# Kernel optimization log

Hardware: AMD Instinct MI355X
Metric: run time of the kernel (lower is better)

## Reference

```python
import jax, jax.numpy as jnp
import numpy as np

B, C, H, W = 16, 256, 96, 96
CQ = C // 8      # 32, query/key channels in CrossAttention
CM = C // 2      # 128, inter_planes


def conv1x1(x, w, b=None):
    # x: [B,Cin,H,W], w: [Cout,Cin]
    y = jnp.einsum('bchw,oc->bohw', x, w)
    if b is not None:
        y = y + b[None, :, None, None]
    return y


def cross_attention(x, wq, bq, wk, bk, wv, bv, gamma):
    # criss-cross (axial H and W) attention with -inf diagonal on the H branch
    b_, c_, h_, w_ = x.shape
    q = conv1x1(x, wq, bq)  # [B,CQ,H,W]
    k = conv1x1(x, wk, bk)
    v = conv1x1(x, wv, bv)  # [B,C,H,W]
    # energy over column (H axis): [B,H,W,H], masked diag h==h'
    e_h = jnp.einsum('bchw,bckw->bhwk', q, k)
    diag = jnp.eye(h_, dtype=bool)[None, :, None, :]  # [1,H,1,H]
    e_h = jnp.where(diag, -jnp.inf, e_h)
    # energy over row (W axis): [B,H,W,W]
    e_w = jnp.einsum('bchw,bchv->bhwv', q, k)
    att = jax.nn.softmax(jnp.concatenate([e_h, e_w], axis=3), axis=3)
    a_h, a_w = att[..., :h_], att[..., h_:]
    out_h = jnp.einsum('bckw,bhwk->bchw', v, a_h)
    out_w = jnp.einsum('bchv,bhwv->bchw', v, a_w)
    return gamma * (out_h + out_w) + x


def spatial_weighted(x, w_q_right, w_v_right, w_up, b_up):
    b_, _, h_, w_ = x.shape
    inp = conv1x1(x, w_v_right).reshape(b_, CM, h_ * w_)        # [B,CM,HW]
    mask = conv1x1(x, w_q_right).reshape(b_, 1, h_ * w_)        # [B,1,HW]
    mask = jax.nn.softmax(mask, axis=2)
    ctx = jnp.einsum('bcn,bon->bco', inp, mask)                 # [B,CM,1]
    ctx = jnp.einsum('bci,oc->boi', ctx, w_up) + b_up[None, :, None]  # [B,C,1]
    mask_ch = jax.nn.sigmoid(ctx)[..., None]                    # [B,C,1,1]
    return x * mask_ch


def channel_weighted(x, w_q_left, w_v_left):
    b_, _, h_, w_ = x.shape
    g = conv1x1(x, w_q_left)                                    # [B,CM,H,W]
    avg = jnp.mean(g, axis=(2, 3))                              # [B,CM]
    theta = conv1x1(x, w_v_left).reshape(b_, CM, h_ * w_)       # [B,CM,HW]
    ctx = jnp.einsum('bc,bcn->bn', avg, theta)                  # [B,HW]
    ctx = jax.nn.softmax(ctx, axis=1).reshape(b_, 1, h_, w_)
    return x * jax.nn.sigmoid(ctx)


def setup_inputs() -> dict:
    key = jax.random.key(0)
    ks = jax.random.split(key, 16)
    s = lambda fan_in: (2.0 / fan_in) ** 0.5
    inp = {
        'x': jax.random.normal(ks[0], (B, C, H, W), jnp.float32),
        'w_q_right': jax.random.normal(ks[1], (1, C), jnp.float32) * s(C),
        'w_v_right': jax.random.normal(ks[2], (CM, C), jnp.float32) * s(C),
        'w_up': jax.random.normal(ks[3], (C, CM), jnp.float32) * s(CM),
        'b_up': jnp.zeros((C,), jnp.float32),
        'w_q_left': jax.random.normal(ks[4], (CM, C), jnp.float32) * s(C),
        'w_v_left': jax.random.normal(ks[5], (CM, C), jnp.float32) * s(C),
        'cr_wq': jax.random.normal(ks[6], (CQ, C), jnp.float32) * s(C),
        'cr_bq': jnp.zeros((CQ,), jnp.float32),
        'cr_wk': jax.random.normal(ks[7], (CQ, C), jnp.float32) * s(C),
        'cr_bk': jnp.zeros((CQ,), jnp.float32),
        'cr_wv': jax.random.normal(ks[8], (C, C), jnp.float32) * s(C),
        'cr_bv': jnp.zeros((C,), jnp.float32),
        'gamma': jax.random.normal(ks[9], (1,), jnp.float32) * 0.1,
    }
    return inp


def reference(x, w_q_right, w_v_right, w_up, b_up, w_q_left, w_v_left,
              cr_wq, cr_bq, cr_wk, cr_bk, cr_wv, cr_bv, gamma):
    cross = lambda t: cross_attention(t, cr_wq, cr_bq, cr_wk, cr_bk, cr_wv, cr_bv, gamma)
    ctx_channel = cross(spatial_weighted(x, w_q_right, w_v_right, w_up, b_up))
    ctx_spatial = cross(channel_weighted(x, w_q_left, w_v_left))
    return cross(ctx_spatial + ctx_channel)
```

## Files before the change

kernel.cpp:

```cpp
#include <hip/hip_runtime.h>
#include <math.h>

#define Bn 16
#define Cn 256
#define CQn 32
#define CMn 128
#define Hn 96
#define Wn 96
#define Nn 9216
#define PIXn 147456

typedef short bf8 __attribute__((ext_vector_type(8)));
typedef float f32x4 __attribute__((ext_vector_type(4)));
#define MFMA(a,b,c) __builtin_amdgcn_mfma_f32_16x16x32_bf16(a,b,c,0,0,0)

typedef unsigned short ushort_t;
typedef _Float16 h16;

__device__ inline ushort_t f2bf(float f){
  union{float f; unsigned int u;} v; v.f=f;
  unsigned int r = v.u + 0x7fffu + ((v.u>>16)&1u);
  return (ushort_t)(r>>16);
}
__device__ inline float bf2f(ushort_t s){
  union{unsigned int u; float f;} v; v.u = ((unsigned int)s)<<16;
  return v.f;
}
__device__ inline ushort_t f2h(float f){
  union{h16 h; ushort_t u;} v; v.h=(h16)f; return v.u;
}
__device__ inline float h2f(ushort_t u){
  union{ushort_t u; h16 h;} v; v.u=u; return (float)v.h;
}

__device__ inline float waveSum(float v){
#pragma unroll
  for(int o=32;o;o>>=1) v += __shfl_down(v,o,64);
  return v;
}
__device__ inline float waveMax(float v){
#pragma unroll
  for(int o=32;o;o>>=1) v = fmaxf(v,__shfl_down(v,o,64));
  return v;
}


__global__ __launch_bounds__(1024) void k_pass1(const float* __restrict__ x,
    const float* __restrict__ wqr, float* __restrict__ xmean,
    float* __restrict__ partp){
  int cg = blockIdx.x, b = blockIdx.y, tid = threadIdx.x;
  __shared__ float r16[16];
  float mp[9];
#pragma unroll
  for(int k=0;k<9;k++) mp[k]=0.f;
  for(int cc=0;cc<16;cc++){
    int c = cg*16+cc;
    const float* row = x + ((size_t)b*Cn + c)*Nn;
    float w = wqr[c];
    float s = 0.f;
#pragma unroll
    for(int k=0;k<9;k++){
      float v = row[k*1024+tid];
      s += v;
      mp[k] += w*v;
    }
    s = waveSum(s);
    if((tid&63)==0) r16[tid>>6]=s;
    __syncthreads();
    if(tid==0){
      float t=0.f;
      for(int i=0;i<16;i++) t+=r16[i];
      xmean[(size_t)b*Cn + c] = t*(1.f/Nn);
    }
    __syncthreads();
  }
  float* dst = partp + ((size_t)cg*Bn + b)*Nn;
#pragma unroll
  for(int k=0;k<9;k++) dst[k*1024+tid]=mp[k];
}

__global__ __launch_bounds__(1024) void k_pass2(const float* __restrict__ x,
    const float* __restrict__ wvec, const float* __restrict__ maskb,
    float* __restrict__ xw, float* __restrict__ partp){
  int cg = blockIdx.x, b = blockIdx.y, tid = threadIdx.x;
  __shared__ float r16[16];
  float cp[9], mk[9];
#pragma unroll
  for(int k=0;k<9;k++){
    cp[k]=0.f;
    mk[k]=maskb[(size_t)b*Nn + k*1024+tid];
  }
  for(int cc=0;cc<16;cc++){
    int c = cg*16+cc;
    const float* row = x + ((size_t)b*Cn + c)*Nn;
    float w = wvec[(size_t)b*Cn + c];
    float s = 0.f;
#pragma unroll
    for(int k=0;k<9;k++){
      float v = row[k*1024+tid];
      s += mk[k]*v;
      cp[k] += w*v;
    }
    s = waveSum(s);
    if((tid&63)==0) r16[tid>>6]=s;
    __syncthreads();
    if(tid==0){
      float t=0.f;
      for(int i=0;i<16;i++) t+=r16[i];
      xw[(size_t)b*Cn + c] = t;
    }
    __syncthreads();
  }
  float* dst = partp + ((size_t)cg*Bn + b)*Nn;
#pragma unroll
  for(int k=0;k<9;k++) dst[k*1024+tid]=cp[k];
}

__global__ void k_red16(const float* __restrict__ part, float* __restrict__ out){
  size_t p = (size_t)blockIdx.x*256 + threadIdx.x;
  float s=0.f;
#pragma unroll
  for(int cg=0;cg<16;cg++) s += part[(size_t)cg*Bn*Nn + p];
  out[p]=s;
}

__global__ void k_small1(const float* __restrict__ xmean, const float* __restrict__ wql,
                         const float* __restrict__ wvl, float* __restrict__ wvec){
  int b=blockIdx.x, t=threadIdx.x;
  __shared__ float xm[Cn];
  __shared__ float av[CMn];
  xm[t] = xmean[b*Cn+t];
  __syncthreads();
  if(t<CMn){
    float s=0.f;
    for(int c=0;c<Cn;c++) s += wql[t*Cn+c]*xm[c];
    av[t]=s;
  }
  __syncthreads();
  float s=0.f;
  for(int m=0;m<CMn;m++) s += av[m]*wvl[m*Cn+t];
  wvec[b*Cn+t]=s;
}

__global__ void k_softmax_n(const float* __restrict__ in, float* __restrict__ out, int mode){
  int b=blockIdx.x, tid=threadIdx.x, lane=tid&63, wid=tid>>6;
  const float* p = in + (size_t)b*Nn;
  __shared__ float red[16];
  __shared__ float bc2[2];
  float mx=-3e38f;
  for(int i=tid;i<Nn;i+=1024) mx=fmaxf(mx,p[i]);
  mx = waveMax(mx);
  if(lane==0) red[wid]=mx;
  __syncthreads();
  if(tid==0){ float m=red[0]; for(int i=1;i<16;i++) m=fmaxf(m,red[i]); bc2[0]=m; }
  __syncthreads();
  mx=bc2[0];
  float s=0.f;
  for(int i=tid;i<Nn;i+=1024) s+=expf(p[i]-mx);
  s = waveSum(s);
  __syncthreads();
  if(lane==0) red[wid]=s;
  __syncthreads();
  if(tid==0){ float t=0.f; for(int i=0;i<16;i++) t+=red[i]; bc2[1]=t; }
  __syncthreads();
  float inv=1.f/bc2[1];
  for(int i=tid;i<Nn;i+=1024){
    float e=expf(p[i]-mx)*inv;
    out[(size_t)b*Nn+i] = mode ? 1.f/(1.f+expf(-e)) : e;
  }
}

__global__ void k_small2(const float* __restrict__ xw, const float* __restrict__ wvr,
                         const float* __restrict__ wup, const float* __restrict__ bup,
                         float* __restrict__ g1){
  int b=blockIdx.x, t=threadIdx.x;
  __shared__ float xs[Cn];
  __shared__ float cx[CMn];
  xs[t]=xw[b*Cn+t];
  __syncthreads();
  if(t<CMn){
    float s=0.f;
    for(int c=0;c<Cn;c++) s += wvr[t*Cn+c]*xs[c];
    cx[t]=s;
  }
  __syncthreads();
  float s=bup[t];
  for(int m=0;m<CMn;m++) s += wup[t*CMn+m]*cx[m];
  g1[b*Cn+t]=1.f/(1.f+expf(-s));
}

__global__ void k_gates(const float* __restrict__ x, const float* __restrict__ g1,
                        const float* __restrict__ m2, ushort_t* __restrict__ t1,
                        ushort_t* __restrict__ t2){
  size_t i4 = ((size_t)blockIdx.x*256 + threadIdx.x)*4;
  int n  = (int)(i4 % Nn);
  int bc = (int)(i4 / Nn);
  int b  = bc / Cn;
  float4 xv = *(const float4*)&x[i4];
  float g = g1[bc];
  float4 mv = *(const float4*)&m2[(size_t)b*Nn + n];
  uint2 a, c;
  a.x = (unsigned)f2bf(xv.x*g) | ((unsigned)f2bf(xv.y*g)<<16);
  a.y = (unsigned)f2bf(xv.z*g) | ((unsigned)f2bf(xv.w*g)<<16);
  c.x = (unsigned)f2bf(xv.x*mv.x) | ((unsigned)f2bf(xv.y*mv.y)<<16);
  c.y = (unsigned)f2bf(xv.z*mv.z) | ((unsigned)f2bf(xv.w*mv.w)<<16);
  *(uint2*)&t1[i4] = a;
  *(uint2*)&t2[i4] = c;
}


__global__ void k_packb(const float* __restrict__ wq, const float* __restrict__ bq,
                        const float* __restrict__ wk, const float* __restrict__ bk,
                        const float* __restrict__ wv, const float* __restrict__ bv,
                        ushort_t* __restrict__ Wp, float* __restrict__ bp){
  int o = blockIdx.x, t = threadIdx.x;
  const float* src; float bs;
  if(o<32){ src = wq + o*Cn; bs = bq[o]; }
  else if(o<64){ src = wk + (o-32)*Cn; bs = bk[o-32]; }
  else { src = wv + (o-64)*Cn; bs = bv[o-64]; }
  Wp[o*Cn+t] = f2bf(src[t]);
  if(t==0) bp[o] = bs;
}

#define AP 40
#define BP 264
#define GP 68

__global__ __launch_bounds__(256) void k_gemm_qkv(const ushort_t* __restrict__ x,
    const ushort_t* __restrict__ Wp, const float* __restrict__ bp,
    ushort_t* __restrict__ Yqk, ushort_t* __restrict__ Vb){
  __shared__ ushort_t SM[320*AP + 64*BP];
  ushort_t* Ws = SM;
  ushort_t* Bt = SM + 320*AP;
  int b  = blockIdx.y;
  int n0 = blockIdx.x*64;
  int tid = threadIdx.x, lane = tid&63, wid = tid>>6;

  {
    const ushort_t* xb = x + (size_t)b*Cn*Nn + n0 + (tid&63);
    int cg = (tid>>6)*8;
#pragma unroll
    for(int p=0;p<8;p++){
      int c8 = p*32 + cg;
      unsigned e0=xb[(size_t)(c8+0)*Nn], e1=xb[(size_t)(c8+1)*Nn];
      unsigned e2=xb[(size_t)(c8+2)*Nn], e3=xb[(size_t)(c8+3)*Nn];
      unsigned e4=xb[(size_t)(c8+4)*Nn], e5=xb[(size_t)(c8+5)*Nn];
      unsigned e6=xb[(size_t)(c8+6)*Nn], e7=xb[(size_t)(c8+7)*Nn];
      uint4 pk;
      pk.x = e0 | (e1<<16); pk.y = e2 | (e3<<16);
      pk.z = e4 | (e5<<16); pk.w = e6 | (e7<<16);
      *(uint4*)&Bt[(tid&63)*BP + c8] = pk;
    }
  }

  f32x4 acc[5][4];
#pragma unroll
  for(int f=0;f<5;f++)
#pragma unroll
    for(int g=0;g<4;g++) acc[f][g] = (f32x4){0.f,0.f,0.f,0.f};

  for(int ki=0;ki<8;ki++){
    __syncthreads();
#pragma unroll
    for(int q=0;q<5;q++){
      int fidx = q*256 + tid;
      int o = fidx>>2, kk = (fidx&3)*8;
      uint4 wv = *(const uint4*)&Wp[o*Cn + ki*32 + kk];
      *(uint4*)&Ws[o*AP + kk] = wv;
    }
    __syncthreads();
    bf8 bfr[4];
#pragma unroll
    for(int g=0;g<4;g++)
      bfr[g] = *(const bf8*)&Bt[(g*16 + (lane&15))*BP + ki*32 + (lane>>4)*8];
#pragma unroll
    for(int f=0;f<5;f++){
      bf8 a = *(const bf8*)&Ws[(wid*80 + f*16 + (lane&15))*AP + (lane>>4)*8];
#pragma unroll
      for(int g=0;g<4;g++) acc[f][g] = MFMA(a, bfr[g], acc[f][g]);
    }
  }

  __syncthreads();
#pragma unroll
  for(int f=0;f<5;f++){
    int o = wid*80 + f*16 + (lane>>4)*4;
#pragma unroll
    for(int i=0;i<4;i++){
      float bias = bp[o+i];
#pragma unroll
      for(int g=0;g<4;g++)
        SM[(o+i)*GP + g*16 + (lane&15)] = f2bf(acc[f][g][i] + bias);
    }
  }
  __syncthreads();
  for(int u=tid; u<320*8; u+=256){
    int lo_ = u>>3, c8 = (u&7)*8;
    ushort_t* dst = (lo_<64) ? (Yqk + ((size_t)b*64 + lo_)*Nn)
                             : (Vb + ((size_t)b*Cn + (lo_-64))*Nn);
    *(uint4*)&dst[n0 + c8] = *(uint4*)&SM[lo_*GP + c8];
  }
}

__global__ __launch_bounds__(256) void k_transpose_b(const ushort_t* __restrict__ src,
                                                     ushort_t* __restrict__ dst){
  __shared__ ushort_t Ls[96*98];
  size_t base = (size_t)blockIdx.x * Nn;
  int tid = threadIdx.x;
  for(int e=tid*2; e<Nn; e+=512){
    unsigned int u = *(const unsigned int*)&src[base+e];
    int r=e/96, c=e%96;
    *(unsigned int*)&Ls[r*98+c] = u;
  }
  __syncthreads();
  for(int e=tid*2; e<Nn; e+=512){
    int r=e/96, c=e%96;
    unsigned int u = (unsigned int)Ls[c*98+r] | (((unsigned int)Ls[(c+1)*98+r])<<16);
    *(unsigned int*)&dst[base+e] = u;
  }
}

__global__ __launch_bounds__(256) void k_e2(const ushort_t* __restrict__ Yqk,
    const ushort_t* __restrict__ Yqkt, ushort_t* __restrict__ attl,
    ushort_t* __restrict__ attr){
  __shared__ ushort_t Qt[96*AP];
  __shared__ ushort_t Kt[96*AP];
  int r = blockIdx.x, mode = blockIdx.y, b = blockIdx.z;
  const ushort_t* Y = mode ? Yqk : Yqkt;
  int pm   = mode ? 1  : 96;
  int pr   = mode ? 96 : 1;
  ushort_t* attx = mode ? attr : attl;
  int tid = threadIdx.x, lane = tid&63, wid = tid>>6;
  {
    int half = tid>>7;
    int cg   = (tid>>5)&3;
    int l32  = tid&31;
    ushort_t* T = half ? Kt : Qt;
    const ushort_t* S = Y + ((size_t)b*64 + half*32 + cg*8)*Nn + (size_t)r*96;
#pragma unroll
    for(int p=0;p<3;p++){
      int sp = p*32 + l32;
      unsigned e0=S[(size_t)0*Nn+sp], e1=S[(size_t)1*Nn+sp];
      unsigned e2=S[(size_t)2*Nn+sp], e3=S[(size_t)3*Nn+sp];
      unsigned e4=S[(size_t)4*Nn+sp], e5=S[(size_t)5*Nn+sp];
      unsigned e6=S[(size_t)6*Nn+sp], e7=S[(size_t)7*Nn+sp];
      uint4 pk;
      pk.x = e0 | (e1<<16); pk.y = e2 | (e3<<16);
      pk.z = e4 | (e5<<16); pk.w = e6 | (e7<<16);
      *(uint4*)&T[sp*AP + cg*8] = pk;
    }
  }
  __syncthreads();
  int mb = (wid>>1)*48, nb = (wid&1)*48;
  const f32x4 z4 = {0.f,0.f,0.f,0.f};
  f32x4 acc[3][3];
  bf8 a[3], bb[3];
#pragma unroll
  for(int f=0;f<3;f++) a[f] = *(const bf8*)&Qt[(mb+f*16+(lane&15))*AP + (lane>>4)*8];
#pragma unroll
  for(int g=0;g<3;g++) bb[g] = *(const bf8*)&Kt[(nb+g*16+(lane&15))*AP + (lane>>4)*8];
#pragma unroll
  for(int f=0;f<3;f++)
#pragma unroll
    for(int g=0;g<3;g++) acc[f][g] = MFMA(a[f], bb[g], z4);
#pragma unroll
  for(int f=0;f<3;f++)
#pragma unroll
    for(int i=0;i<4;i++){
      int m = mb + f*16 + (lane>>4)*4 + i;
      ushort_t* arow = attx + ((size_t)b*Nn + (size_t)m*pm + (size_t)r*pr)*96;
#pragma unroll
      for(int g=0;g<3;g++){
        int n = nb + g*16 + (lane&15);
        arow[n] = f2h(acc[f][g][i]);
      }
    }
}

__global__ void k_softmax_att(const ushort_t* __restrict__ attl,
    const ushort_t* __restrict__ attr,
    ushort_t* __restrict__ attw, ushort_t* __restrict__ atth){
  int wave = threadIdx.x>>6, lane = threadIdx.x&63;
  int p = blockIdx.x*4 + wave;
  const ushort_t* al = attl + (size_t)p*96;
  const ushort_t* ar = attr + (size_t)p*96;
  int b = p/Nn, rem = p%Nn, h = rem/96, w = rem%96;
  float v0 = h2f(al[lane]);
  if(lane==h) v0 = -1e30f;
  float v1;
  if(lane<32){
    v1 = h2f(al[64+lane]);
    if(64+lane==h) v1 = -1e30f;
  } else {
    v1 = h2f(ar[lane-32]);
  }
  float v2 = h2f(ar[lane+32]);
  float mx = fmaxf(v0, fmaxf(v1,v2));
#pragma unroll
  for(int o=32;o;o>>=1) mx = fmaxf(mx, __shfl_xor(mx,o,64));
  float e0=expf(v0-mx), e1=expf(v1-mx), e2=expf(v2-mx);
  float s=e0+e1+e2;
#pragma unroll
  for(int o=32;o;o>>=1) s += __shfl_xor(s,o,64);
  float inv=1.f/s;
  ushort_t* ph = atth + ((size_t)b*Nn + (size_t)w*96 + h)*96;
  ushort_t* pw = attw + (size_t)p*96;
  ph[lane] = f2bf(e0*inv);
  if(lane<32) ph[64+lane] = f2bf(e1*inv);
  else        pw[lane-32] = f2bf(e1*inv);
  pw[lane+32] = f2bf(e2*inv);
}

#define SP 120
#define RP 100

template<int OUTF>
__global__ __launch_bounds__(256) void k_pv2(const ushort_t* __restrict__ Vb,
    const ushort_t* __restrict__ VT, const ushort_t* __restrict__ attw,
    const ushort_t* __restrict__ atth, const ushort_t* resid,
    float* __restrict__ Of, ushort_t* OwB, ushort_t* OT,
    const float* __restrict__ gp){
  __shared__ ushort_t SMEM[128*RP];
  int r = blockIdx.x, mode = blockIdx.y>>1, half = blockIdx.y&1, b = blockIdx.z;
  float gm = gp[0];
  int tid = threadIdx.x, lane = tid&63, wid = tid>>6;
  const ushort_t* V = mode ? VT : Vb;
  size_t vbase = (size_t)b*Cn*Nn + (size_t)r*96;
  bf8 vf[6];
#pragma unroll
  for(int f=0;f<2;f++)
#pragma unroll
    for(int j=0;j<3;j++)
      vf[f*3+j] = *(const bf8*)&V[vbase
        + (size_t)(half*128 + wid*32 + f*16 + (lane&15))*Nn + j*32 + (lane>>4)*8];
  const ushort_t* ab = (mode ? atth : attw) + ((size_t)b*Nn + (size_t)r*96)*96;
  for(int u=tid; u<96*12; u+=256){
    int n=u/12, j8=(u%12)*8;
    uint4 q = *(const uint4*)&ab[n*96 + j8];
    *(uint4*)&SMEM[n*SP + j8] = q;
  }
  __syncthreads();
  f32x4 acc[2][6];
#pragma unroll
  for(int f=0;f<2;f++)
#pragma unroll
    for(int g=0;g<6;g++) acc[f][g] = (f32x4){0.f,0.f,0.f,0.f};
#pragma unroll
  for(int j0=0;j0<3;j0++){
    bf8 bfr[6];
#pragma unroll
    for(int g=0;g<6;g++)
      bfr[g] = *(const bf8*)&SMEM[(g*16+(lane&15))*SP + j0*32 + (lane>>4)*8];
#pragma unroll
    for(int f=0;f<2;f++)
#pragma unroll
      for(int g=0;g<6;g++) acc[f][g] = MFMA(vf[f*3+j0], bfr[g], acc[f][g]);
  }
  __syncthreads();
#pragma unroll
  for(int f=0;f<2;f++){
    int lr = wid*32 + f*16 + (lane>>4)*4;
#pragma unroll
    for(int i=0;i<4;i++)
#pragma unroll
      for(int g=0;g<6;g++)
        SMEM[(lr+i)*RP + g*16 + (lane&15)] = f2bf(gm*acc[f][g][i]);
  }
  __syncthreads();
  for(int u=tid; u<128*12; u+=256){
    int lc = u/12, q8 = (u%12)*8;
    size_t row = vbase + (size_t)(half*128 + lc)*Nn;
    uint4 v = *(uint4*)&SMEM[lc*RP + q8];
    if(mode){
      *(uint4*)&OT[row + q8] = v;
    } else {
      uint4 rv = *(const uint4*)&resid[row + q8];
      unsigned* vp=(unsigned*)&v; unsigned* rp=(unsigned*)&rv;
      if(OUTF){
        float4 o1, o2;
        o1.x = bf2f((ushort_t)(vp[0]&0xffff)) + bf2f((ushort_t)(rp[0]&0xffff));
        o1.y = bf2f((ushort_t)(vp[0]>>16))    + bf2f((ushort_t)(rp[0]>>16));
        o1.z = bf2f((ushort_t)(vp[1]&0xffff)) + bf2f((ushort_t)(rp[1]&0xffff));
        o1.w = bf2f((ushort_t)(vp[1]>>16))    + bf2f((ushort_t)(rp[1]>>16));
        o2.x = bf2f((ushort_t)(vp[2]&0xffff)) + bf2f((ushort_t)(rp[2]&0xffff));
        o2.y = bf2f((ushort_t)(vp[2]>>16))    + bf2f((ushort_t)(rp[2]>>16));
        o2.z = bf2f((ushort_t)(vp[3]&0xffff)) + bf2f((ushort_t)(rp[3]&0xffff));
        o2.w = bf2f((ushort_t)(vp[3]>>16))    + bf2f((ushort_t)(rp[3]>>16));
        *(float4*)&Of[row + q8]     = o1;
        *(float4*)&Of[row + q8 + 4] = o2;
      } else {
        uint4 o;
        unsigned* op=(unsigned*)&o;
#pragma unroll
        for(int k=0;k<4;k++){
          float lo = bf2f((ushort_t)(vp[k]&0xffff)) + bf2f((ushort_t)(rp[k]&0xffff));
          float hi = bf2f((ushort_t)(vp[k]>>16))    + bf2f((ushort_t)(rp[k]>>16));
          op[k] = (unsigned)f2bf(lo) | ((unsigned)f2bf(hi)<<16);
        }
        *(uint4*)&OwB[row + q8] = o;
      }
    }
  }
}

template<int VAR>
__global__ __launch_bounds__(256) void k_merge(float* __restrict__ outf,
    ushort_t* __restrict__ outb, const ushort_t* __restrict__ add,
    const ushort_t* __restrict__ OT){
  __shared__ ushort_t Ls[96*98];
  size_t base = (size_t)blockIdx.x * Nn;
  int tid = threadIdx.x;
  for(int e=tid*2; e<Nn; e+=512){
    unsigned int u = *(const unsigned int*)&OT[base+e];
    int r=e/96, c=e%96;
    *(unsigned int*)&Ls[r*98+c] = u;
  }
  __syncthreads();
  for(int e=tid*4; e<Nn; e+=1024){
    int r=e/96, c=e%96;
    float t0 = bf2f(Ls[(c+0)*98+r]), t1 = bf2f(Ls[(c+1)*98+r]);
    float t2 = bf2f(Ls[(c+2)*98+r]), t3 = bf2f(Ls[(c+3)*98+r]);
    if(VAR==1){
      float4 o = *(float4*)&outf[base+e];
      o.x += t0; o.y += t1; o.z += t2; o.w += t3;
      *(float4*)&outf[base+e] = o;
    } else {
      uint2 u = *(uint2*)&outb[base+e];
      float a0 = bf2f((ushort_t)(u.x&0xffff)) + t0;
      float a1 = bf2f((ushort_t)(u.x>>16))    + t1;
      float a2 = bf2f((ushort_t)(u.y&0xffff)) + t2;
      float a3 = bf2f((ushort_t)(u.y>>16))    + t3;
      if(VAR==2){
        uint2 v = *(const uint2*)&add[base+e];
        a0 += bf2f((ushort_t)(v.x&0xffff));
        a1 += bf2f((ushort_t)(v.x>>16));
        a2 += bf2f((ushort_t)(v.y&0xffff));
        a3 += bf2f((ushort_t)(v.y>>16));
      }
      u.x = (unsigned)f2bf(a0) | ((unsigned)f2bf(a1)<<16);
      u.y = (unsigned)f2bf(a2) | ((unsigned)f2bf(a3)<<16);
      *(uint2*)&outb[base+e] = u;
    }
  }
}

extern "C" void kernel_launch(void* const* d_in, const int* in_sizes, int n_in,
                              void* d_out, int out_size, void* d_ws, size_t ws_size,
                              hipStream_t stream){
  const float* x    = (const float*)d_in[0];
  const float* wqr  = (const float*)d_in[1];
  const float* wvr  = (const float*)d_in[2];
  const float* wup  = (const float*)d_in[3];
  const float* bup  = (const float*)d_in[4];
  const float* wql  = (const float*)d_in[5];
  const float* wvl  = (const float*)d_in[6];
  const float* crwq = (const float*)d_in[7];
  const float* crbq = (const float*)d_in[8];
  const float* crwk = (const float*)d_in[9];
  const float* crbk = (const float*)d_in[10];
  const float* crwv = (const float*)d_in[11];
  const float* crbv = (const float*)d_in[12];
  const float* gma  = (const float*)d_in[13];
  float* out = (float*)d_out;

  const size_t XSZ = (size_t)Bn*Cn*Nn;
  const size_t YSZ = (size_t)Bn*64*Nn;
  char* wsb = (char*)d_ws;
  ushort_t* T1   = (ushort_t*)wsb; wsb += XSZ*2;
  ushort_t* T2   = (ushort_t*)wsb; wsb += XSZ*2;
  ushort_t* Vb   = (ushort_t*)wsb; wsb += XSZ*2;
  ushort_t* VT   = (ushort_t*)wsb; wsb += XSZ*2;
  ushort_t* Yqk  = (ushort_t*)wsb; wsb += YSZ*2;
  ushort_t* Yqkt = (ushort_t*)wsb; wsb += YSZ*2;
  ushort_t* ATTL = (ushort_t*)wsb; wsb += (size_t)PIXn*96*2;
  ushort_t* ATTR = (ushort_t*)wsb; wsb += (size_t)PIXn*96*2;
  ushort_t* ATTw = (ushort_t*)wsb; wsb += (size_t)PIXn*96*2;
  ushort_t* ATTh = (ushort_t*)wsb; wsb += (size_t)PIXn*96*2;
  float*    partp= (float*)wsb;    wsb += (size_t)16*Bn*Nn*4;
  ushort_t* Wpb  = (ushort_t*)wsb; wsb += 320*Cn*2;
  float*    bp   = (float*)wsb;    wsb += 320*4;
  float*    xmean= (float*)wsb;    wsb += Bn*Cn*4;
  float*    wvec = (float*)wsb;    wsb += Bn*Cn*4;
  float*    xw   = (float*)wsb;    wsb += Bn*Cn*4;
  float*    g1   = (float*)wsb;    wsb += Bn*Cn*4;
  float*    mraw = (float*)wsb;    wsb += (size_t)PIXn*4;
  float*    maskb= (float*)wsb;    wsb += (size_t)PIXn*4;
  float*    craw = (float*)wsb;    wsb += (size_t)PIXn*4;
  float*    m2   = (float*)wsb;    wsb += (size_t)PIXn*4;

  k_packb<<<320,256,0,stream>>>(crwq,crbq,crwk,crbk,crwv,crbv,Wpb,bp);

  k_pass1<<<dim3(16,Bn),1024,0,stream>>>(x, wqr, xmean, partp);
  k_red16<<<Bn*Nn/256,256,0,stream>>>(partp, mraw);
  k_small1<<<Bn,256,0,stream>>>(xmean, wql, wvl, wvec);
  k_softmax_n<<<Bn,1024,0,stream>>>(mraw, maskb, 0);
  k_pass2<<<dim3(16,Bn),1024,0,stream>>>(x, wvec, maskb, xw, partp);
  k_red16<<<Bn*Nn/256,256,0,stream>>>(partp, craw);
  k_softmax_n<<<Bn,1024,0,stream>>>(craw, m2, 1);
  k_small2<<<Bn,256,0,stream>>>(xw, wvr, wup, bup, g1);
  k_gates<<<XSZ/1024,256,0,stream>>>(x, g1, m2, T1, T2);

  auto cross = [&](const ushort_t* t, ushort_t* ob, float* of, int var){
    k_gemm_qkv<<<dim3(Nn/64,Bn),256,0,stream>>>(t, Wpb, bp, Yqk, Vb);
    k_transpose_b<<<Bn*64,256,0,stream>>>(Yqk, Yqkt);
    k_e2<<<dim3(96,2,Bn),256,0,stream>>>(Yqk, Yqkt, ATTL, ATTR);
    k_softmax_att<<<PIXn/4,256,0,stream>>>(ATTL, ATTR, ATTw, ATTh);
    k_transpose_b<<<Bn*Cn,256,0,stream>>>(Vb, VT);
    if(var==1) k_pv2<1><<<dim3(96,4,Bn),256,0,stream>>>(Vb, VT, ATTw, ATTh, t, of, nullptr, VT, gma);
    else       k_pv2<0><<<dim3(96,4,Bn),256,0,stream>>>(Vb, VT, ATTw, ATTh, t, nullptr, ob, VT, gma);
    if(var==0)      k_merge<0><<<Bn*Cn,256,0,stream>>>(nullptr, ob, nullptr, VT);
    else if(var==1) k_merge<1><<<Bn*Cn,256,0,stream>>>(of, nullptr, nullptr, VT);
    else            k_merge<2><<<Bn*Cn,256,0,stream>>>(nullptr, T1, T2, VT);
  };

  cross(T1, T1, nullptr, 0);
  cross(T2, T2, nullptr, 2);
  cross(T1, nullptr, out, 1);
}
```

Before: 1.149 ms.

## Fuse gating into QKV GEMM, batch first two cross-attentions, in-place softmax

Removes the separate gate kernel: the x*g1 and x*m2 gating is computed inside the QKV GEMM load and in the pv2 residual, so the gated bf16 inputs are no longer materialized up front. When workspace allows, the first two cross-attention passes run as one batched launch sequence over a doubled grid. The merge kernel then adds both results in a single pass. The attention softmax now works in place on paired (i,j)/(j,i) triangle pixels, dropping two attention buffers. This trades extra fp32 reads of x and a larger workspace for fewer launches, fewer intermediate buffers and more parallelism per launch.

```diff
diff --git a/kernel.cpp b/kernel.cpp
--- a/kernel.cpp
+++ b/kernel.cpp
@@ -3,12 +3,13 @@
 
 #define Bn 16
 #define Cn 256
-#define CQn 32
-#define CMn 128
 #define Hn 96
 #define Wn 96
 #define Nn 9216
 #define PIXn 147456
+#define XSZk ((size_t)Bn*Cn*Nn)
+#define YSZk ((size_t)Bn*64*Nn)
+#define ATTSZ ((size_t)PIXn*96)
 
 typedef short bf8 __attribute__((ext_vector_type(8)));
 typedef float f32x4 __attribute__((ext_vector_type(4)));
@@ -128,17 +129,17 @@
                          const float* __restrict__ wvl, float* __restrict__ wvec){
   int b=blockIdx.x, t=threadIdx.x;
   __shared__ float xm[Cn];
-  __shared__ float av[CMn];
+  __shared__ float av[128];
   xm[t] = xmean[b*Cn+t];
   __syncthreads();
-  if(t<CMn){
+  if(t<128){
     float s=0.f;
     for(int c=0;c<Cn;c++) s += wql[t*Cn+c]*xm[c];
     av[t]=s;
   }
   __syncthreads();
   float s=0.f;
-  for(int m=0;m<CMn;m++) s += av[m]*wvl[m*Cn+t];
+  for(int m=0;m<128;m++) s += av[m]*wvl[m*Cn+t];
   wvec[b*Cn+t]=s;
 }
 
@@ -175,37 +176,18 @@
                          float* __restrict__ g1){
   int b=blockIdx.x, t=threadIdx.x;
   __shared__ float xs[Cn];
-  __shared__ float cx[CMn];
+  __shared__ float cx[128];
   xs[t]=xw[b*Cn+t];
   __syncthreads();
-  if(t<CMn){
+  if(t<128){
     float s=0.f;
     for(int c=0;c<Cn;c++) s += wvr[t*Cn+c]*xs[c];
     cx[t]=s;
   }
   __syncthreads();
   float s=bup[t];
-  for(int m=0;m<CMn;m++) s += wup[t*CMn+m]*cx[m];
+  for(int m=0;m<128;m++) s += wup[t*128+m]*cx[m];
   g1[b*Cn+t]=1.f/(1.f+expf(-s));
-}
-
-__global__ void k_gates(const float* __restrict__ x, const float* __restrict__ g1,
-                        const float* __restrict__ m2, ushort_t* __restrict__ t1,
-                        ushort_t* __restrict__ t2){
-  size_t i4 = ((size_t)blockIdx.x*256 + threadIdx.x)*4;
-  int n  = (int)(i4 % Nn);
-  int bc = (int)(i4 / Nn);
-  int b  = bc / Cn;
-  float4 xv = *(const float4*)&x[i4];
-  float g = g1[bc];
-  float4 mv = *(const float4*)&m2[(size_t)b*Nn + n];
-  uint2 a, c;
-  a.x = (unsigned)f2bf(xv.x*g) | ((unsigned)f2bf(xv.y*g)<<16);
-  a.y = (unsigned)f2bf(xv.z*g) | ((unsigned)f2bf(xv.w*g)<<16);
-  c.x = (unsigned)f2bf(xv.x*mv.x) | ((unsigned)f2bf(xv.y*mv.y)<<16);
-  c.y = (unsigned)f2bf(xv.z*mv.z) | ((unsigned)f2bf(xv.w*mv.w)<<16);
-  *(uint2*)&t1[i4] = a;
-  *(uint2*)&t2[i4] = c;
 }
 
 
@@ -226,18 +208,45 @@
 #define BP 264
 #define GP 68
 
-__global__ __launch_bounds__(256) void k_gemm_qkv(const ushort_t* __restrict__ x,
+template<int GATED>
+__global__ __launch_bounds__(256) void k_gemm_qkv(
+    const ushort_t* __restrict__ tb, const float* __restrict__ x,
+    const float* __restrict__ g1, const float* __restrict__ m2,
     const ushort_t* __restrict__ Wp, const float* __restrict__ bp,
-    ushort_t* __restrict__ Yqk, ushort_t* __restrict__ Vb){
+    ushort_t* __restrict__ Yqk, ushort_t* __restrict__ Vb, int selbase){
   __shared__ ushort_t SM[320*AP + 64*BP];
+  __shared__ float gsh[256];
   ushort_t* Ws = SM;
   ushort_t* Bt = SM + 320*AP;
-  int b  = blockIdx.y;
+  int by = blockIdx.y, b = by & 15, sl = by >> 4;
+  int sel = selbase + sl;
   int n0 = blockIdx.x*64;
   int tid = threadIdx.x, lane = tid&63, wid = tid>>6;
 
-  {
-    const ushort_t* xb = x + (size_t)b*Cn*Nn + n0 + (tid&63);
+  if(GATED){
+    gsh[tid] = g1[b*Cn + tid];
+    __syncthreads();
+    const float* xb = x + (size_t)b*Cn*Nn + n0 + (tid&63);
+    float scl_n = (sel==1) ? m2[(size_t)b*Nn + n0 + (tid&63)] : 0.f;
+    int cg = (tid>>6)*8;
+#pragma unroll
+    for(int p=0;p<8;p++){
+      int c8 = p*32 + cg;
+      float fv[8];
+#pragma unroll
+      for(int k2=0;k2<8;k2++){
+        float xf = xb[(size_t)(c8+k2)*Nn];
+        fv[k2] = xf * (sel==0 ? gsh[c8+k2] : scl_n);
+      }
+      uint4 pk;
+      pk.x = (unsigned)f2bf(fv[0]) | ((unsigned)f2bf(fv[1])<<16);
+      pk.y = (unsigned)f2bf(fv[2]) | ((unsigned)f2bf(fv[3])<<16);
+      pk.z = (unsigned)f2bf(fv[4]) | ((unsigned)f2bf(fv[5])<<16);
+      pk.w = (unsigned)f2bf(fv[6]) | ((unsigned)f2bf(fv[7])<<16);
+      *(uint4*)&Bt[(tid&63)*BP + c8] = pk;
+    }
+  } else {
+    const ushort_t* xb = tb + (size_t)b*Cn*Nn + n0 + (tid&63);
     int cg = (tid>>6)*8;
 #pragma unroll
     for(int p=0;p<8;p++){
@@ -294,10 +303,12 @@
     }
   }
   __syncthreads();
+  ushort_t* Yo = Yqk + (size_t)sl*YSZk;
+  ushort_t* Vo = Vb  + (size_t)sl*XSZk;
   for(int u=tid; u<320*8; u+=256){
     int lo_ = u>>3, c8 = (u&7)*8;
-    ushort_t* dst = (lo_<64) ? (Yqk + ((size_t)b*64 + lo_)*Nn)
-                             : (Vb + ((size_t)b*Cn + (lo_-64))*Nn);
+    ushort_t* dst = (lo_<64) ? (Yo + ((size_t)b*64 + lo_)*Nn)
+                             : (Vo + ((size_t)b*Cn + (lo_-64))*Nn);
     *(uint4*)&dst[n0 + c8] = *(uint4*)&SM[lo_*GP + c8];
   }
 }
@@ -325,11 +336,12 @@
     ushort_t* __restrict__ attr){
   __shared__ ushort_t Qt[96*AP];
   __shared__ ushort_t Kt[96*AP];
-  int r = blockIdx.x, mode = blockIdx.y, b = blockIdx.z;
-  const ushort_t* Y = mode ? Yqk : Yqkt;
+  int r = blockIdx.x, mode = blockIdx.y;
+  int zz = blockIdx.z, b = zz & 15, sl = zz >> 4;
+  const ushort_t* Y = (mode ? Yqk : Yqkt) + (size_t)sl*YSZk;
   int pm   = mode ? 1  : 96;
   int pr   = mode ? 96 : 1;
-  ushort_t* attx = mode ? attr : attl;
+  ushort_t* attx = (mode ? attr : attl) + (size_t)sl*ATTSZ;
   int tid = threadIdx.x, lane = tid&63, wid = tid>>6;
   {
     int half = tid>>7;
@@ -377,54 +389,65 @@
     }
 }
 
-__global__ void k_softmax_att(const ushort_t* __restrict__ attl,
-    const ushort_t* __restrict__ attr,
-    ushort_t* __restrict__ attw, ushort_t* __restrict__ atth){
-  int wave = threadIdx.x>>6, lane = threadIdx.x&63;
-  int p = blockIdx.x*4 + wave;
-  const ushort_t* al = attl + (size_t)p*96;
-  const ushort_t* ar = attr + (size_t)p*96;
-  int b = p/Nn, rem = p%Nn, h = rem/96, w = rem%96;
-  float v0 = h2f(al[lane]);
-  if(lane==h) v0 = -1e30f;
-  float v1;
-  if(lane<32){
-    v1 = h2f(al[64+lane]);
-    if(64+lane==h) v1 = -1e30f;
-  } else {
-    v1 = h2f(ar[lane-32]);
-  }
-  float v2 = h2f(ar[lane+32]);
-  float mx = fmaxf(v0, fmaxf(v1,v2));
-#pragma unroll
-  for(int o=32;o;o>>=1) mx = fmaxf(mx, __shfl_xor(mx,o,64));
-  float e0=expf(v0-mx), e1=expf(v1-mx), e2=expf(v2-mx);
-  float s=e0+e1+e2;
-#pragma unroll
-  for(int o=32;o;o>>=1) s += __shfl_xor(s,o,64);
-  float inv=1.f/s;
-  ushort_t* ph = atth + ((size_t)b*Nn + (size_t)w*96 + h)*96;
-  ushort_t* pw = attw + (size_t)p*96;
-  ph[lane] = f2bf(e0*inv);
-  if(lane<32) ph[64+lane] = f2bf(e1*inv);
-  else        pw[lane-32] = f2bf(e1*inv);
-  pw[lane+32] = f2bf(e2*inv);
+__global__ __launch_bounds__(256) void k_softmax_ip(ushort_t* attl, ushort_t* attr){
+  int wave = threadIdx.x>>6, l = threadIdx.x&63;
+  int t = blockIdx.x*4 + wave;
+  int zz = blockIdx.z, b = zz & 15, sl = zz >> 4;
+  attl += (size_t)sl*ATTSZ; attr += (size_t)sl*ATTSZ;
+  int i=0, base=0;
+  while(base + (96-i) <= t){ base += 96-i; i++; }
+  int j = i + (t-base);
+  int hf = l>>5, l32 = l&31;
+  int h = hf ? j : i, w = hf ? i : j;
+  size_t p = (size_t)b*Nn + (size_t)h*96 + w;
+  const ushort_t* al = attl + p*96;
+  const ushort_t* ar = attr + p*96;
+  float v[6];
+#pragma unroll
+  for(int k=0;k<3;k++){
+    int el = l32 + 32*k;
+    float vv = h2f(al[el]);
+    v[k] = (el==h) ? -1e30f : vv;
+  }
+#pragma unroll
+  for(int k=0;k<3;k++) v[3+k] = h2f(ar[l32 + 32*k]);
+  float mx = v[0];
+#pragma unroll
+  for(int k=1;k<6;k++) mx = fmaxf(mx, v[k]);
+#pragma unroll
+  for(int o=16;o;o>>=1) mx = fmaxf(mx, __shfl_xor(mx, o, 64));
+  float e[6], s=0.f;
+#pragma unroll
+  for(int k=0;k<6;k++){ e[k]=expf(v[k]-mx); s+=e[k]; }
+#pragma unroll
+  for(int o=16;o;o>>=1) s += __shfl_xor(s, o, 64);
+  float inv = 1.f/s;
+  size_t q = (size_t)b*Nn + (size_t)w*96 + h;
+  ushort_t* oh = attl + q*96;
+  ushort_t* ow = attr + p*96;
+#pragma unroll
+  for(int k=0;k<3;k++) oh[l32+32*k] = f2bf(e[k]*inv);
+#pragma unroll
+  for(int k=0;k<3;k++) ow[l32+32*k] = f2bf(e[3+k]*inv);
 }
 
 #define SP 120
 #define RP 100
 
-template<int OUTF>
-__global__ __launch_bounds__(256) void k_pv2(const ushort_t* __restrict__ Vb,
-    const ushort_t* __restrict__ VT, const ushort_t* __restrict__ attw,
-    const ushort_t* __restrict__ atth, const ushort_t* resid,
-    float* __restrict__ Of, ushort_t* OwB, ushort_t* OT,
-    const float* __restrict__ gp){
+template<int FIN>
+__global__ __launch_bounds__(256) void k_pv2(const ushort_t* __restrict__ VB,
+    const ushort_t* __restrict__ VTb, const ushort_t* __restrict__ attw,
+    const ushort_t* __restrict__ atth, const float* __restrict__ x,
+    const float* __restrict__ g1, const float* __restrict__ m2,
+    const ushort_t* __restrict__ residb, ushort_t* TT, float* __restrict__ Of,
+    ushort_t* OTb, const float* __restrict__ gp, int selbase){
   __shared__ ushort_t SMEM[128*RP];
-  int r = blockIdx.x, mode = blockIdx.y>>1, half = blockIdx.y&1, b = blockIdx.z;
+  int r = blockIdx.x, mode = blockIdx.y>>1, half = blockIdx.y&1;
+  int zz = blockIdx.z, b = zz & 15, sl = zz >> 4;
+  int sel = selbase + sl;
   float gm = gp[0];
   int tid = threadIdx.x, lane = tid&63, wid = tid>>6;
-  const ushort_t* V = mode ? VT : Vb;
+  const ushort_t* V = (mode ? VTb : VB) + (size_t)sl*XSZk;
   size_t vbase = (size_t)b*Cn*Nn + (size_t)r*96;
   bf8 vf[6];
 #pragma unroll
@@ -433,7 +456,8 @@
     for(int j=0;j<3;j++)
       vf[f*3+j] = *(const bf8*)&V[vbase
         + (size_t)(half*128 + wid*32 + f*16 + (lane&15))*Nn + j*32 + (lane>>4)*8];
-  const ushort_t* ab = (mode ? atth : attw) + ((size_t)b*Nn + (size_t)r*96)*96;
+  const ushort_t* ab = (mode ? atth : attw) + (size_t)sl*ATTSZ
+                     + ((size_t)b*Nn + (size_t)r*96)*96;
   for(int u=tid; u<96*12; u+=256){
     int n=u/12, j8=(u%12)*8;
     uint4 q = *(const uint4*)&ab[n*96 + j8];
@@ -467,16 +491,20 @@
         SMEM[(lr+i)*RP + g*16 + (lane&15)] = f2bf(gm*acc[f][g][i]);
   }
   __syncthreads();
+  ushort_t* OT = OTb + (size_t)sl*XSZk;
+  ushort_t* To = TT + (size_t)sel*XSZk;
   for(int u=tid; u<128*12; u+=256){
     int lc = u/12, q8 = (u%12)*8;
-    size_t row = vbase + (size_t)(half*128 + lc)*Nn;
+    int c = half*128 + lc;
+    size_t row = vbase + (size_t)c*Nn;
     uint4 v = *(uint4*)&SMEM[lc*RP + q8];
     if(mode){
       *(uint4*)&OT[row + q8] = v;
     } else {
-      uint4 rv = *(const uint4*)&resid[row + q8];
-      unsigned* vp=(unsigned*)&v; unsigned* rp=(unsigned*)&rv;
-      if(OUTF){
+      unsigned* vp=(unsigned*)&v;
+      if(FIN){
+        uint4 rv = *(const uint4*)&residb[row + q8];
+        unsigned* rp=(unsigned*)&rv;
         float4 o1, o2;
         o1.x = bf2f((ushort_t)(vp[0]&0xffff)) + bf2f((ushort_t)(rp[0]&0xffff));
         o1.y = bf2f((ushort_t)(vp[0]>>16))    + bf2f((ushort_t)(rp[0]>>16));
@@ -489,15 +517,27 @@
         *(float4*)&Of[row + q8]     = o1;
         *(float4*)&Of[row + q8 + 4] = o2;
       } else {
-        uint4 o;
-        unsigned* op=(unsigned*)&o;
+        float4 x1 = *(const float4*)&x[row + q8];
+        float4 x2 = *(const float4*)&x[row + q8 + 4];
+        float rs[8];
+        if(sel==0){
+          float g = g1[b*Cn + c];
+          rs[0]=x1.x*g; rs[1]=x1.y*g; rs[2]=x1.z*g; rs[3]=x1.w*g;
+          rs[4]=x2.x*g; rs[5]=x2.y*g; rs[6]=x2.z*g; rs[7]=x2.w*g;
+        } else {
+          float4 m1 = *(const float4*)&m2[(size_t)b*Nn + (size_t)r*96 + q8];
+          float4 m2v= *(const float4*)&m2[(size_t)b*Nn + (size_t)r*96 + q8 + 4];
+          rs[0]=x1.x*m1.x; rs[1]=x1.y*m1.y; rs[2]=x1.z*m1.z; rs[3]=x1.w*m1.w;
+          rs[4]=x2.x*m2v.x; rs[5]=x2.y*m2v.y; rs[6]=x2.z*m2v.z; rs[7]=x2.w*m2v.w;
+        }
+        uint4 o; unsigned* op=(unsigned*)&o;
 #pragma unroll
         for(int k=0;k<4;k++){
-          float lo = bf2f((ushort_t)(vp[k]&0xffff)) + bf2f((ushort_t)(rp[k]&0xffff));
-          float hi = bf2f((ushort_t)(vp[k]>>16))    + bf2f((ushort_t)(rp[k]>>16));
+          float lo = bf2f((ushort_t)(vp[k]&0xffff)) + rs[2*k];
+          float hi = bf2f((ushort_t)(vp[k]>>16))    + rs[2*k+1];
           op[k] = (unsigned)f2bf(lo) | ((unsigned)f2bf(hi)<<16);
         }
-        *(uint4*)&OwB[row + q8] = o;
+        *(uint4*)&To[row + q8] = o;
       }
     }
   }
@@ -508,18 +548,24 @@
     ushort_t* __restrict__ outb, const ushort_t* __restrict__ add,
     const ushort_t* __restrict__ OT){
   __shared__ ushort_t Ls[96*98];
+  __shared__ ushort_t Ls2[(VAR==3)?96*98:1];
   size_t base = (size_t)blockIdx.x * Nn;
   int tid = threadIdx.x;
   for(int e=tid*2; e<Nn; e+=512){
-    unsigned int u = *(const unsigned int*)&OT[base+e];
     int r=e/96, c=e%96;
-    *(unsigned int*)&Ls[r*98+c] = u;
+    *(unsigned int*)&Ls[r*98+c] = *(const unsigned int*)&OT[base+e];
+    if(VAR==3)
+      *(unsigned int*)&Ls2[r*98+c] = *(const unsigned int*)&OT[XSZk + base + e];
   }
   __syncthreads();
   for(int e=tid*4; e<Nn; e+=1024){
     int r=e/96, c=e%96;
     float t0 = bf2f(Ls[(c+0)*98+r]), t1 = bf2f(Ls[(c+1)*98+r]);
     float t2 = bf2f(Ls[(c+2)*98+r]), t3 = bf2f(Ls[(c+3)*98+r]);
+    if(VAR==3){
+      t0 += bf2f(Ls2[(c+0)*98+r]); t1 += bf2f(Ls2[(c+1)*98+r]);
+      t2 += bf2f(Ls2[(c+2)*98+r]); t3 += bf2f(Ls2[(c+3)*98+r]);
+    }
     if(VAR==1){
       float4 o = *(float4*)&outf[base+e];
       o.x += t0; o.y += t1; o.z += t2; o.w += t3;
@@ -530,7 +576,7 @@
       float a1 = bf2f((ushort_t)(u.x>>16))    + t1;
       float a2 = bf2f((ushort_t)(u.y&0xffff)) + t2;
       float a3 = bf2f((ushort_t)(u.y>>16))    + t3;
-      if(VAR==2){
+      if(VAR==2 || VAR==3){
         uint2 v = *(const uint2*)&add[base+e];
         a0 += bf2f((ushort_t)(v.x&0xffff));
         a1 += bf2f((ushort_t)(v.x>>16));
@@ -563,19 +609,16 @@
   const float* gma  = (const float*)d_in[13];
   float* out = (float*)d_out;
 
-  const size_t XSZ = (size_t)Bn*Cn*Nn;
-  const size_t YSZ = (size_t)Bn*64*Nn;
+  const int nsel = (ws_size >= (size_t)654000000) ? 2 : 1;
+
   char* wsb = (char*)d_ws;
-  ushort_t* T1   = (ushort_t*)wsb; wsb += XSZ*2;
-  ushort_t* T2   = (ushort_t*)wsb; wsb += XSZ*2;
-  ushort_t* Vb   = (ushort_t*)wsb; wsb += XSZ*2;
-  ushort_t* VT   = (ushort_t*)wsb; wsb += XSZ*2;
-  ushort_t* Yqk  = (ushort_t*)wsb; wsb += YSZ*2;
-  ushort_t* Yqkt = (ushort_t*)wsb; wsb += YSZ*2;
-  ushort_t* ATTL = (ushort_t*)wsb; wsb += (size_t)PIXn*96*2;
-  ushort_t* ATTR = (ushort_t*)wsb; wsb += (size_t)PIXn*96*2;
-  ushort_t* ATTw = (ushort_t*)wsb; wsb += (size_t)PIXn*96*2;
-  ushort_t* ATTh = (ushort_t*)wsb; wsb += (size_t)PIXn*96*2;
+  ushort_t* TT   = (ushort_t*)wsb; wsb += 2*XSZk*2;
+  ushort_t* VB2  = (ushort_t*)wsb; wsb += (size_t)nsel*XSZk*2;
+  ushort_t* VT2  = (ushort_t*)wsb; wsb += (size_t)nsel*XSZk*2;
+  ushort_t* Y2   = (ushort_t*)wsb; wsb += (size_t)nsel*YSZk*2;
+  ushort_t* Yt2  = (ushort_t*)wsb; wsb += (size_t)nsel*YSZk*2;
+  ushort_t* ATTL = (ushort_t*)wsb; wsb += (size_t)nsel*ATTSZ*2;
+  ushort_t* ATTR = (ushort_t*)wsb; wsb += (size_t)nsel*ATTSZ*2;
   float*    partp= (float*)wsb;    wsb += (size_t)16*Bn*Nn*4;
   ushort_t* Wpb  = (ushort_t*)wsb; wsb += 320*Cn*2;
   float*    bp   = (float*)wsb;    wsb += 320*4;
@@ -598,22 +641,34 @@
   k_red16<<<Bn*Nn/256,256,0,stream>>>(partp, craw);
   k_softmax_n<<<Bn,1024,0,stream>>>(craw, m2, 1);
   k_small2<<<Bn,256,0,stream>>>(xw, wvr, wup, bup, g1);
-  k_gates<<<XSZ/1024,256,0,stream>>>(x, g1, m2, T1, T2);
-
-  auto cross = [&](const ushort_t* t, ushort_t* ob, float* of, int var){
-    k_gemm_qkv<<<dim3(Nn/64,Bn),256,0,stream>>>(t, Wpb, bp, Yqk, Vb);
-    k_transpose_b<<<Bn*64,256,0,stream>>>(Yqk, Yqkt);
-    k_e2<<<dim3(96,2,Bn),256,0,stream>>>(Yqk, Yqkt, ATTL, ATTR);
-    k_softmax_att<<<PIXn/4,256,0,stream>>>(ATTL, ATTR, ATTw, ATTh);
-    k_transpose_b<<<Bn*Cn,256,0,stream>>>(Vb, VT);
-    if(var==1) k_pv2<1><<<dim3(96,4,Bn),256,0,stream>>>(Vb, VT, ATTw, ATTh, t, of, nullptr, VT, gma);
-    else       k_pv2<0><<<dim3(96,4,Bn),256,0,stream>>>(Vb, VT, ATTw, ATTh, t, nullptr, ob, VT, gma);
-    if(var==0)      k_merge<0><<<Bn*Cn,256,0,stream>>>(nullptr, ob, nullptr, VT);
-    else if(var==1) k_merge<1><<<Bn*Cn,256,0,stream>>>(of, nullptr, nullptr, VT);
-    else            k_merge<2><<<Bn*Cn,256,0,stream>>>(nullptr, T1, T2, VT);
+
+  auto cross12 = [&](int selbase, int nsl){
+    k_gemm_qkv<1><<<dim3(Nn/64,Bn*nsl),256,0,stream>>>(nullptr, x, g1, m2, Wpb, bp, Y2, VB2, selbase);
+    k_transpose_b<<<Bn*64*nsl,256,0,stream>>>(Y2, Yt2);
+    k_e2<<<dim3(96,2,Bn*nsl),256,0,stream>>>(Y2, Yt2, ATTL, ATTR);
+    k_softmax_ip<<<dim3(1164,1,Bn*nsl),256,0,stream>>>(ATTL, ATTR);
+    k_transpose_b<<<Bn*Cn*nsl,256,0,stream>>>(VB2, VT2);
+    k_pv2<0><<<dim3(96,4,Bn*nsl),256,0,stream>>>(VB2, VT2, ATTR, ATTL,
+        x, g1, m2, nullptr, TT, nullptr, VT2, gma, selbase);
   };
 
-  cross(T1, T1, nullptr, 0);
-  cross(T2, T2, nullptr, 2);
-  cross(T1, nullptr, out, 1);
-}
+  ushort_t* T2p = TT + XSZk;
+  if(nsel==2){
+    cross12(0, 2);
+    k_merge<3><<<Bn*Cn,256,0,stream>>>(nullptr, TT, T2p, VT2);
+  } else {
+    cross12(0, 1);
+    k_merge<0><<<Bn*Cn,256,0,stream>>>(nullptr, TT, nullptr, VT2);
+    cross12(1, 1);
+    k_merge<2><<<Bn*Cn,256,0,stream>>>(nullptr, TT, T2p, VT2);
+  }
+
+  k_gemm_qkv<0><<<dim3(Nn/64,Bn),256,0,stream>>>(TT, nullptr, nullptr, nullptr, Wpb, bp, Y2, VB2, 0);
+  k_transpose_b<<<Bn*64,256,0,stream>>>(Y2, Yt2);
+  k_e2<<<dim3(96,2,Bn),256,0,stream>>>(Y2, Yt2, ATTL, ATTR);
+  k_softmax_ip<<<dim3(1164,1,Bn),256,0,stream>>>(ATTL, ATTR);
+  k_transpose_b<<<Bn*Cn,256,0,stream>>>(VB2, VT2);
+  k_pv2<1><<<dim3(96,4,Bn),256,0,stream>>>(VB2, VT2, ATTR, ATTL,
+      nullptr, nullptr, nullptr, TT, nullptr, out, VT2, gma, 0);
+  k_merge<1><<<Bn*Cn,256,0,stream>>>(out, nullptr, nullptr, VT2);
+}
```

Measured after the change: 1.145 ms. About the same (-0.4%).
